# Optimization experiments

Hardware: AMD Instinct MI355X
Metric: run time of the kernel (lower is better)

Reference implementation:

```python
import jax, jax.numpy as jnp
import numpy as np

C = 1024
R = 4            # reduction
A = 10           # num_adapters
LN_EPS = 1e-5
THRESHOLDS = np.array([1/9, 1/7, 1/5, 1/3, 1.0, 3.0, 5.0, 7.0, 9.0], dtype=np.float32)


def setup_inputs() -> dict:
    key = jax.random.key(0)
    k_feat, k_ar, k_w1, k_w2 = jax.random.split(key, 4)
    B, NA, H, W = 2, 3, 64, 64
    Cr = C // R
    output_feat = jax.random.normal(k_feat, (B, C, H, W), jnp.float32)
    # aspect ratios in [0,10) so all 10 adapters get selected
    aspect_ratio = jax.random.uniform(k_ar, (B, NA, H, W), jnp.float32) * 10.0
    # LayerNorm params (torch default init: weight=1, bias=0), stacked over adapters
    ln_scale = jnp.ones((A, C), jnp.float32)
    ln_bias = jnp.zeros((A, C), jnp.float32)
    # kaiming_normal_ fan_out / relu: std = sqrt(2/fan_out); torch weight [out,in]
    # w1 here is [C, Cr] == torch weight [Cr, C].T, fan_out = Cr
    w1 = jax.random.normal(k_w1, (A, C, Cr), jnp.float32) * np.sqrt(2.0 / Cr)
    # w2 here is [Cr, C] == torch weight [C, Cr].T, fan_out = C
    w2 = jax.random.normal(k_w2, (A, Cr, C), jnp.float32) * np.sqrt(2.0 / C)
    return dict(output_feat=output_feat, aspect_ratio=aspect_ratio,
                ln_scale=ln_scale, ln_bias=ln_bias, w1=w1, w2=w2)


def reference(output_feat, aspect_ratio, ln_scale, ln_bias, w1, w2):
    B, Cc, H, W = output_feat.shape
    NA = aspect_ratio.shape[1]
    HW = H * W
    # tokens [N, C]
    x = output_feat.transpose(0, 2, 3, 1).reshape(-1, Cc)
    # shared LayerNorm normalization (per-adapter affine applied after)
    mu = jnp.mean(x, axis=-1, keepdims=True)
    var = jnp.var(x, axis=-1, keepdims=True)
    norm = (x - mu) * jax.lax.rsqrt(var + LN_EPS)              # [N, C]
    y = norm[None, :, :] * ln_scale[:, None, :] + ln_bias[:, None, :]  # [A, N, C]
    h = jax.nn.gelu(jnp.einsum('anc,acd->and', y, w1), approximate=False)
    adapter_out = jnp.einsum('and,adc->anc', h, w2)            # [A, N, C]
    adapter_out = adapter_out.reshape(A, B, HW, Cc)            # [A, B, HW, C]
    # per-anchor, per-pixel adapter index from aspect ratio vs thresholds
    thr = jnp.asarray(THRESHOLDS, dtype=aspect_ratio.dtype)
    ar = aspect_ratio.reshape(B, NA, HW)
    idx = jnp.sum(ar[..., None] > thr, axis=-1)                # [B, NA, HW] in [0, 9]
    # gather selected adapter output per (batch, anchor, pixel)
    b_idx = jnp.arange(B)[:, None, None]
    p_idx = jnp.arange(HW)[None, None, :]
    selected = adapter_out[idx, b_idx, p_idx]                  # [B, NA, HW, C]
    selected = selected.mean(axis=1).reshape(B, H, W, Cc).transpose(0, 3, 1, 2)
    return selected + output_feat
```

## Files before the change

### kernel.cpp

```cpp
#include <hip/hip_runtime.h>
#include <hip/hip_bf16.h>
#include <math.h>

#define C_DIM 1024
#define CR    256
#define A_N   10
#define NANCH 3
#define B_N   2
#define HW_N  4096
#define NTOK  (B_N*HW_N)
#define KG2   (A_N*CR)

typedef unsigned short ushort_t;
typedef __attribute__((ext_vector_type(4))) float f32x4;
typedef __attribute__((ext_vector_type(8))) short bf16x8;

__device__ __forceinline__ ushort_t f2bf(float x) {
    __hip_bfloat16 h = __float2bfloat16(x);
    return *reinterpret_cast<ushort_t*>(&h);
}
__device__ __forceinline__ float bf2f(ushort_t u) {
    return __uint_as_float(((unsigned)u) << 16);
}

__device__ __forceinline__ float fast_gelu(float x) {
    float t = x * x;
    float u = x * (-1.5957691216f - 0.0713548163f * t);
    float e = __expf(u);
    return x * __frcp_rn(1.0f + e);
}

__global__ __launch_bounds__(256) void prep_all(
    const float* __restrict__ w1, const float* __restrict__ w2,
    const float* __restrict__ ln_s, const float* __restrict__ ln_b,
    const float* __restrict__ feat, const float* __restrict__ ar,
    ushort_t* __restrict__ w1t, ushort_t* __restrict__ w2t,
    float* __restrict__ bias1, float* __restrict__ cs1,
    float* __restrict__ sumv, float* __restrict__ sumq,
    int* __restrict__ cnt, int* __restrict__ tokw, int* __restrict__ tokmap,
    ushort_t* __restrict__ featT) {
    __shared__ float lds[64][65];
    __shared__ float bb[8][64];
    __shared__ int lcnt[A_N], lpos[A_N], gbase[A_N];
    int id = blockIdx.x, tid = threadIdx.x;
    int lo = tid & 63, hi = tid >> 6;

    if (id < 640) {
        int d0 = (id & 3) * 64, c0 = ((id >> 2) & 15) * 64, a = id >> 6;
        #pragma unroll
        for (int i = 0; i < 16; i++) {
            int c_l = i * 4 + hi;
            lds[c_l][lo] = w1[((size_t)a * C_DIM + c0 + c_l) * CR + d0 + lo];
        }
        __syncthreads();
        {
            float s = 0.f, s2 = 0.f;
            #pragma unroll
            for (int cc = 0; cc < 16; cc++) {
                int c = hi * 16 + cc;
                float v = lds[c][lo];
                s  += v * ln_b[a * C_DIM + c0 + c];
                s2 += v * ln_s[a * C_DIM + c0 + c];
            }
            bb[hi][lo] = s;
            bb[hi + 4][lo] = s2;
        }
        float sc = ln_s[a * C_DIM + c0 + lo];
        #pragma unroll
        for (int i = 0; i < 16; i++) {
            int d_l = i * 4 + hi;
            w1t[((size_t)a * CR + d0 + d_l) * C_DIM + c0 + lo] = f2bf(lds[lo][d_l] * sc);
        }
        __syncthreads();
        if (hi == 0)
            atomicAdd(&bias1[a * CR + d0 + lo], bb[0][lo] + bb[1][lo] + bb[2][lo] + bb[3][lo]);
        else if (hi == 1)
            atomicAdd(&cs1[a * CR + d0 + lo], bb[4][lo] + bb[5][lo] + bb[6][lo] + bb[7][lo]);
    } else if (id < 1280) {
        int id2 = id - 640;
        int k0 = (id2 % 40) * 64, c0 = (id2 / 40) * 64;
        #pragma unroll
        for (int i = 0; i < 16; i++) {
            int k_l = i * 4 + hi;
            lds[k_l][lo] = w2[((size_t)k0 + k_l) * C_DIM + c0 + lo];
        }
        __syncthreads();
        #pragma unroll
        for (int i = 0; i < 16; i++) {
            int c_l = i * 4 + hi;
            w2t[((size_t)c0 + c_l) * KG2 + k0 + lo] = f2bf(lds[lo][c_l]);
        }
    } else if (id < 3328) {
        int id2 = id - 1280;
        int p0 = (id2 & 63) * 64, c0 = ((id2 >> 6) & 15) * 64, b = id2 >> 10;
        #pragma unroll
        for (int i = 0; i < 16; i++) {
            int c_l = i * 4 + hi;
            lds[c_l][lo] = feat[((size_t)b * C_DIM + c0 + c_l) * HW_N + p0 + lo];
        }
        __syncthreads();
        {
            float s = 0.f, s2 = 0.f;
            #pragma unroll
            for (int c = hi; c < 64; c += 4) {
                float v = lds[c][lo];
                s += v; s2 += v * v;
            }
            bb[hi][lo] = s; bb[hi + 4][lo] = s2;
        }
        __syncthreads();
        if (tid < 64) {
            float ss = bb[0][tid] + bb[1][tid] + bb[2][tid] + bb[3][tid];
            float qq = bb[4][tid] + bb[5][tid] + bb[6][tid] + bb[7][tid];
            int t = b * HW_N + p0 + tid;
            atomicAdd(&sumv[t], ss);
            atomicAdd(&sumq[t], qq);
        }
        int t_l = tid >> 3, cg = tid & 7;
        #pragma unroll
        for (int ii = 0; ii < 2; ii++) {
            int tl = ii * 32 + t_l;
            bf16x8 v;
            #pragma unroll
            for (int k = 0; k < 8; k++)
                v[k] = (short)f2bf(lds[cg * 8 + k][tl]);
            *(bf16x8*)(featT + (size_t)(b * HW_N + p0 + tl) * C_DIM + c0 + cg * 8) = v;
        }
    } else {
        if (tid < A_N) { lcnt[tid] = 0; lpos[tid] = 0; }
        __syncthreads();
        int t = (id - 3328) * 256 + tid;
        int b = t >> 12, p = t & (HW_N - 1);
        const float THR[9] = {1.0f/9.0f, 1.0f/7.0f, 0.2f, 1.0f/3.0f, 1.0f, 3.0f, 5.0f, 7.0f, 9.0f};
        int idxs[NANCH];
        #pragma unroll
        for (int na = 0; na < NANCH; na++) {
            float v = ar[(size_t)b * NANCH * HW_N + na * HW_N + p];
            int idx = 0;
            #pragma unroll
            for (int i = 0; i < 9; i++) idx += (v > THR[i]) ? 1 : 0;
            idxs[na] = idx;
        }
        int myA[NANCH], myC[NANCH], nmine = 0;
        #pragma unroll
        for (int j = 0; j < NANCH; j++) {
            bool first = true; int c3 = 0;
            #pragma unroll
            for (int k = 0; k < NANCH; k++) {
                if (idxs[k] == idxs[j]) { c3++; if (k < j) first = false; }
            }
            if (first) {
                myA[nmine] = idxs[j];
                myC[nmine] = c3;
                nmine++;
                atomicAdd(&lcnt[idxs[j]], 1);
            }
        }
        __syncthreads();
        if (tid < A_N) gbase[tid] = atomicAdd(&cnt[tid], lcnt[tid]);
        __syncthreads();
        for (int i = 0; i < NANCH; i++) {
            if (i < nmine) {
                int a2 = myA[i];
                int slot = atomicAdd(&lpos[a2], 1);
                int pos = gbase[a2] + slot;
                tokw[a2 * NTOK + pos] = t;
                tokmap[t * 3 + i] = pos | (a2 << 13) | (myC[i] << 17);
            } else {
                tokmap[t * 3 + i] = 0;
            }
        }
    }
}

__device__ __forceinline__ void gemm_core_ptrs(
    const ushort_t* const ap[4], const ushort_t* const bp[4],
    int K, ushort_t* As, ushort_t* Bs, f32x4 acc[4][4]) {
    const int tid = threadIdx.x;
    const int lane = tid & 63;
    const int w = tid >> 6;
    const int wr = w >> 1, wc = w & 1;
    const int lrow = lane & 15;
    const int quad = lane >> 4;
    const int swzr = lrow & 7;

    #pragma unroll
    for (int i = 0; i < 4; i++)
        #pragma unroll
        for (int j = 0; j < 4; j++)
            #pragma unroll
            for (int e = 0; e < 4; e++) acc[i][j][e] = 0.f;

    for (int k0 = 0; k0 < K; k0 += 64) {
        __syncthreads();
        #pragma unroll
        for (int i = 0; i < 4; i++) {
            __builtin_amdgcn_global_load_lds(
                (__attribute__((address_space(1))) void*)(ap[i] + k0),
                (__attribute__((address_space(3))) void*)(As + (w * 32 + i * 8) * 64),
                16, 0, 0);
            __builtin_amdgcn_global_load_lds(
                (__attribute__((address_space(1))) void*)(bp[i] + k0),
                (__attribute__((address_space(3))) void*)(Bs + (w * 32 + i * 8) * 64),
                16, 0, 0);
        }
        __syncthreads();
        #pragma unroll
        for (int ks = 0; ks < 2; ks++) {
            const int cidx = ((ks * 4 + quad) ^ swzr) * 8;
            bf16x8 af[4], bfr[4];
            #pragma unroll
            for (int mt = 0; mt < 4; mt++)
                af[mt] = *(const bf16x8*)(As + (wr * 64 + mt * 16 + lrow) * 64 + cidx);
            #pragma unroll
            for (int nt = 0; nt < 4; nt++)
                bfr[nt] = *(const bf16x8*)(Bs + (wc * 64 + nt * 16 + lrow) * 64 + cidx);
            #pragma unroll
            for (int mt = 0; mt < 4; mt++)
                #pragma unroll
                for (int nt = 0; nt < 4; nt++)
                    acc[mt][nt] = __builtin_amdgcn_mfma_f32_16x16x32_bf16(af[mt], bfr[nt], acc[mt][nt], 0, 0, 0);
        }
    }
}

__device__ __forceinline__ void gemm_core_bk128(
    const ushort_t* const ap[4], const ushort_t* const bp[4],
    int K, ushort_t* As, ushort_t* Bs, f32x4 acc[4][4]) {
    const int tid = threadIdx.x;
    const int lane = tid & 63;
    const int w = tid >> 6;
    const int wr = w >> 1, wc = w & 1;
    const int lrow = lane & 15;
    const int quad = lane >> 4;
    const int swzr = lrow & 7;

    #pragma unroll
    for (int i = 0; i < 4; i++)
        #pragma unroll
        for (int j = 0; j < 4; j++)
            #pragma unroll
            for (int e = 0; e < 4; e++) acc[i][j][e] = 0.f;

    for (int k0 = 0; k0 < K; k0 += 128) {
        __syncthreads();
        #pragma unroll
        for (int p = 0; p < 2; p++) {
            #pragma unroll
            for (int i = 0; i < 4; i++) {
                __builtin_amdgcn_global_load_lds(
                    (__attribute__((address_space(1))) void*)(ap[i] + k0 + p * 64),
                    (__attribute__((address_space(3))) void*)(As + p * 8192 + (w * 32 + i * 8) * 64),
                    16, 0, 0);
                __builtin_amdgcn_global_load_lds(
                    (__attribute__((address_space(1))) void*)(bp[i] + k0 + p * 64),
                    (__attribute__((address_space(3))) void*)(Bs + p * 8192 + (w * 32 + i * 8) * 64),
                    16, 0, 0);
            }
        }
        __syncthreads();
        #pragma unroll
        for (int ks = 0; ks < 4; ks++) {
            const ushort_t* Ab = As + (ks >> 1) * 8192;
            const ushort_t* Bb = Bs + (ks >> 1) * 8192;
            const int cidx = (((ks & 1) * 4 + quad) ^ swzr) * 8;
            bf16x8 af[4], bfr[4];
            #pragma unroll
            for (int mt = 0; mt < 4; mt++)
                af[mt] = *(const bf16x8*)(Ab + (wr * 64 + mt * 16 + lrow) * 64 + cidx);
            #pragma unroll
            for (int nt = 0; nt < 4; nt++)
                bfr[nt] = *(const bf16x8*)(Bb + (wc * 64 + nt * 16 + lrow) * 64 + cidx);
            #pragma unroll
            for (int mt = 0; mt < 4; mt++)
                #pragma unroll
                for (int nt = 0; nt < 4; nt++)
                    acc[mt][nt] = __builtin_amdgcn_mfma_f32_16x16x32_bf16(af[mt], bfr[nt], acc[mt][nt], 0, 0, 0);
        }
    }
}

__global__ __launch_bounds__(256) void gemm1c(const ushort_t* __restrict__ featT,
                                              const ushort_t* __restrict__ w1t,
                                              const float* __restrict__ bias1,
                                              const float* __restrict__ cs1,
                                              const float* __restrict__ sumv,
                                              const float* __restrict__ sumq,
                                              const int* __restrict__ tokw,
                                              const int* __restrict__ cnt,
                                              ushort_t* __restrict__ Hc) {
    int a = blockIdx.z;
    int mcount = cnt[a];
    int m0 = blockIdx.y * 128;
    if (m0 >= mcount) return;
    int n0 = blockIdx.x * 128;
    int base = 0;
    for (int a2 = 0; a2 < a; a2++) base += cnt[a2];

    __shared__ __align__(16) ushort_t As[2 * 128 * 64];
    __shared__ __align__(16) ushort_t Bs[2 * 128 * 64];

    int tid = threadIdx.x, lane = tid & 63, w = tid >> 6;
    int lrow8 = lane >> 3;
    int scol = ((lane & 7) ^ lrow8) * 8;
    int srowl = w * 32 + lrow8;

    const ushort_t* ap[4];
    const ushort_t* bp[4];
    #pragma unroll
    for (int i = 0; i < 4; i++) {
        int rt = tokw[a * NTOK + m0 + srowl + i * 8] & (NTOK - 1);
        ap[i] = featT + (size_t)rt * C_DIM + scol;
        bp[i] = w1t + ((size_t)a * CR + n0 + srowl + i * 8) * C_DIM + scol;
    }

    f32x4 acc[4][4];
    gemm_core_bk128(ap, bp, C_DIM, As, Bs, acc);

    int wr = w >> 1, wc = w & 1, lrow = lane & 15, quad = lane >> 4;
    float bi[4], cs[4];
    #pragma unroll
    for (int nt = 0; nt < 4; nt++) {
        int col = a * CR + n0 + wc * 64 + nt * 16 + lrow;
        bi[nt] = bias1[col];
        cs[nt] = cs1[col];
    }
    #pragma unroll
    for (int mt = 0; mt < 4; mt++)
        #pragma unroll
        for (int r = 0; r < 4; r++) {
            int i_row = m0 + wr * 64 + mt * 16 + quad * 4 + r;
            bool live = i_row < mcount;
            int t = tokw[a * NTOK + i_row] & (NTOK - 1);
            float m = sumv[t] * (1.f / C_DIM);
            float q = sumq[t] * (1.f / C_DIM);
            float rn = rsqrtf(q - m * m + 1e-5f);
            #pragma unroll
            for (int nt = 0; nt < 4; nt++) {
                int col = n0 + wc * 64 + nt * 16 + lrow;
                float v = rn * (acc[mt][nt][r] - m * cs[nt]) + bi[nt];
                if (live)
                    Hc[(size_t)(base + i_row) * CR + col] = f2bf(fast_gelu(v));
            }
        }
}

__global__ __launch_bounds__(256) void gemm2c(const ushort_t* __restrict__ Hc,
                                              const ushort_t* __restrict__ w2t,
                                              const int* __restrict__ cnt,
                                              ushort_t* __restrict__ O) {
    int a = blockIdx.z;
    int mcount = cnt[a];
    int m0 = blockIdx.y * 128;
    if (m0 >= mcount) return;
    int n0 = blockIdx.x * 128;
    int base = 0;
    for (int a2 = 0; a2 < a; a2++) base += cnt[a2];

    __shared__ __align__(16) ushort_t As[128 * 64];
    __shared__ __align__(16) ushort_t Bs[128 * 64];

    int tid = threadIdx.x, lane = tid & 63, w = tid >> 6;
    int lrow8 = lane >> 3;
    int scol = ((lane & 7) ^ lrow8) * 8;
    int srowl = w * 32 + lrow8;

    const ushort_t* ap[4];
    const ushort_t* bp[4];
    #pragma unroll
    for (int i = 0; i < 4; i++) {
        ap[i] = Hc + (size_t)(base + m0 + srowl + i * 8) * CR + scol;
        bp[i] = w2t + (size_t)(n0 + srowl + i * 8) * KG2 + a * CR + scol;
    }

    f32x4 acc[4][4];
    gemm_core_ptrs(ap, bp, CR, As, Bs, acc);

    int wr = w >> 1, wc = w & 1, lrow = lane & 15, quad = lane >> 4;
    #pragma unroll
    for (int mt = 0; mt < 4; mt++)
        #pragma unroll
        for (int r = 0; r < 4; r++) {
            int i_row = m0 + wr * 64 + mt * 16 + quad * 4 + r;
            bool live = i_row < mcount;
            #pragma unroll
            for (int nt = 0; nt < 4; nt++) {
                int col = n0 + wc * 64 + nt * 16 + lrow;
                if (live)
                    O[(size_t)(base + i_row) * C_DIM + col] = f2bf(acc[mt][nt][r]);
            }
        }
}

__global__ __launch_bounds__(256) void finalk2(const ushort_t* __restrict__ O,
                                               const int* __restrict__ tokmap,
                                               const int* __restrict__ cnt,
                                               const float* __restrict__ feat,
                                               float* __restrict__ out) {
    int p0 = blockIdx.x * 64, c0 = blockIdx.y * 64, b = blockIdx.z;
    __shared__ float lds[64][65];
    __shared__ int pbase[A_N];
    int tid = threadIdx.x, lo = tid & 63, hi = tid >> 6;
    if (tid < A_N) {
        int s = 0;
        for (int k = 0; k < tid; k++) s += cnt[k];
        pbase[tid] = s;
    }
    __syncthreads();
    int t_l = tid >> 3, cg = tid & 7;
    #pragma unroll
    for (int ii = 0; ii < 2; ii++) {
        int tl = ii * 32 + t_l;
        int t = b * HW_N + p0 + tl;
        float val8[8];
        #pragma unroll
        for (int k = 0; k < 8; k++) val8[k] = 0.f;
        #pragma unroll
        for (int j = 0; j < 3; j++) {
            int e = tokmap[t * 3 + j];
            float wv = (float)(e >> 17) * (1.0f / 3.0f);
            int a2 = (e >> 13) & 15;
            int row = pbase[a2] + (e & 8191);
            bf16x8 v = *(const bf16x8*)(O + (size_t)row * C_DIM + c0 + cg * 8);
            #pragma unroll
            for (int k = 0; k < 8; k++)
                val8[k] += wv * bf2f((ushort_t)v[k]);
        }
        #pragma unroll
        for (int k = 0; k < 8; k++)
            lds[tl][cg * 8 + k] = val8[k];
    }
    __syncthreads();
    #pragma unroll
    for (int i = 0; i < 16; i++) {
        int c_l = i * 4 + hi;
        size_t o = ((size_t)b * C_DIM + c0 + c_l) * HW_N + p0 + lo;
        out[o] = lds[lo][c_l] + feat[o];
    }
}

extern "C" void kernel_launch(void* const* d_in, const int* in_sizes, int n_in,
                              void* d_out, int out_size, void* d_ws, size_t ws_size,
                              hipStream_t stream) {
    (void)in_sizes; (void)n_in; (void)out_size; (void)ws_size;
    const float* feat = (const float*)d_in[0];
    const float* ar   = (const float*)d_in[1];
    const float* ln_s = (const float*)d_in[2];
    const float* ln_b = (const float*)d_in[3];
    const float* w1   = (const float*)d_in[4];
    const float* w2   = (const float*)d_in[5];
    float* out = (float*)d_out;
    char* ws = (char*)d_ws;

    float*    bias1  = (float*)(ws + 0);
    float*    cs1    = (float*)(ws + 10240);
    int*      cnt    = (int*)(ws + 20480);
    float*    sumv   = (float*)(ws + 20736);
    float*    sumq   = (float*)(ws + 53504);
    const size_t ZERO_BYTES = 86272;
    int*      tokmap = (int*)(ws + 86272);
    int*      tokw   = (int*)(ws + 184576);
    ushort_t* w1t    = (ushort_t*)(ws + 512256);
    ushort_t* w2t    = (ushort_t*)(ws + 5755136);
    ushort_t* featT  = (ushort_t*)(ws + 10998016);
    ushort_t* Hc     = (ushort_t*)(ws + 27775232);
    ushort_t* O      = (ushort_t*)(ws + 40423680);

    dim3 blk(256);
    hipMemsetAsync(ws, 0, ZERO_BYTES, stream);
    prep_all<<<dim3(3360), blk, 0, stream>>>(w1, w2, ln_s, ln_b, feat, ar,
                                             w1t, w2t, bias1, cs1, sumv, sumq,
                                             cnt, tokw, tokmap, featT);
    gemm1c<<<dim3(2, 64, A_N), blk, 0, stream>>>(featT, w1t, bias1, cs1, sumv, sumq,
                                                 tokw, cnt, Hc);
    gemm2c<<<dim3(8, 64, A_N), blk, 0, stream>>>(Hc, w2t, cnt, O);
    finalk2<<<dim3(64, 16, B_N), blk, 0, stream>>>(O, tokmap, cnt, feat, out);
}
```

Baseline: 95.42 us.

## Replace global atomics with partial-sum buffers and single-block token bucketing; drop memset

Token-to-adapter bucketing now runs in one block that loops over all tokens with only shared-memory atomics, which removes the global counter atomics. Per-token LayerNorm sums and per-column bias/colsum terms are written as 16 partial slots per row or column instead of being accumulated with global atomicAdd. gemm1c reduces those partials into shared memory in its epilogue. The hipMemsetAsync launch goes away, and the partial buffers alias the O buffer, which is written only later. The risk is that the serial single block becomes a long tail inside prep_all, since it walks 8192 tokens alone.

```diff
diff --git a/kernel.cpp b/kernel.cpp
--- a/kernel.cpp
+++ b/kernel.cpp
@@ -35,18 +35,55 @@
     const float* __restrict__ ln_s, const float* __restrict__ ln_b,
     const float* __restrict__ feat, const float* __restrict__ ar,
     ushort_t* __restrict__ w1t, ushort_t* __restrict__ w2t,
-    float* __restrict__ bias1, float* __restrict__ cs1,
-    float* __restrict__ sumv, float* __restrict__ sumq,
+    float* __restrict__ bias1P, float* __restrict__ cs1P,
+    float* __restrict__ sums,
     int* __restrict__ cnt, int* __restrict__ tokw, int* __restrict__ tokmap,
     ushort_t* __restrict__ featT) {
     __shared__ float lds[64][65];
     __shared__ float bb[8][64];
-    __shared__ int lcnt[A_N], lpos[A_N], gbase[A_N];
+    __shared__ int lpos[A_N];
     int id = blockIdx.x, tid = threadIdx.x;
     int lo = tid & 63, hi = tid >> 6;
 
-    if (id < 640) {
-        int d0 = (id & 3) * 64, c0 = ((id >> 2) & 15) * 64, a = id >> 6;
+    if (id == 0) {
+        if (tid < A_N) lpos[tid] = 0;
+        __syncthreads();
+        const float THR[9] = {1.0f/9.0f, 1.0f/7.0f, 0.2f, 1.0f/3.0f, 1.0f, 3.0f, 5.0f, 7.0f, 9.0f};
+        for (int it = 0; it < NTOK / 256; ++it) {
+            int t = it * 256 + tid;
+            int b = t >> 12, p = t & (HW_N - 1);
+            int idxs[NANCH];
+            #pragma unroll
+            for (int na = 0; na < NANCH; na++) {
+                float v = ar[(size_t)b * NANCH * HW_N + na * HW_N + p];
+                int idx = 0;
+                #pragma unroll
+                for (int i = 0; i < 9; i++) idx += (v > THR[i]) ? 1 : 0;
+                idxs[na] = idx;
+            }
+            #pragma unroll
+            for (int j = 0; j < NANCH; j++) {
+                bool first = true; int c3 = 0;
+                #pragma unroll
+                for (int k = 0; k < NANCH; k++) {
+                    if (idxs[k] == idxs[j]) { c3++; if (k < j) first = false; }
+                }
+                int e = 0;
+                if (first) {
+                    int a2 = idxs[j];
+                    int pos = atomicAdd(&lpos[a2], 1);
+                    tokw[a2 * NTOK + pos] = t;
+                    e = pos | (a2 << 13) | (c3 << 17);
+                }
+                tokmap[t * 3 + j] = e;
+            }
+        }
+        __syncthreads();
+        if (tid < A_N) cnt[tid] = lpos[tid];
+    } else if (id < 641) {
+        int id2 = id - 1;
+        int d0 = (id2 & 3) * 64, c0idx = (id2 >> 2) & 15, a = id2 >> 6;
+        int c0 = c0idx * 64;
         #pragma unroll
         for (int i = 0; i < 16; i++) {
             int c_l = i * 4 + hi;
@@ -73,11 +110,13 @@
         }
         __syncthreads();
         if (hi == 0)
-            atomicAdd(&bias1[a * CR + d0 + lo], bb[0][lo] + bb[1][lo] + bb[2][lo] + bb[3][lo]);
+            bias1P[(size_t)(a * CR + d0 + lo) * 16 + c0idx] =
+                bb[0][lo] + bb[1][lo] + bb[2][lo] + bb[3][lo];
         else if (hi == 1)
-            atomicAdd(&cs1[a * CR + d0 + lo], bb[4][lo] + bb[5][lo] + bb[6][lo] + bb[7][lo]);
-    } else if (id < 1280) {
-        int id2 = id - 640;
+            cs1P[(size_t)(a * CR + d0 + lo) * 16 + c0idx] =
+                bb[4][lo] + bb[5][lo] + bb[6][lo] + bb[7][lo];
+    } else if (id < 1281) {
+        int id2 = id - 641;
         int k0 = (id2 % 40) * 64, c0 = (id2 / 40) * 64;
         #pragma unroll
         for (int i = 0; i < 16; i++) {
@@ -90,9 +129,10 @@
             int c_l = i * 4 + hi;
             w2t[((size_t)c0 + c_l) * KG2 + k0 + lo] = f2bf(lds[lo][c_l]);
         }
-    } else if (id < 3328) {
-        int id2 = id - 1280;
-        int p0 = (id2 & 63) * 64, c0 = ((id2 >> 6) & 15) * 64, b = id2 >> 10;
+    } else {
+        int id2 = id - 1281;
+        int p0 = (id2 & 63) * 64, c0idx = (id2 >> 6) & 15, b = id2 >> 10;
+        int c0 = c0idx * 64;
         #pragma unroll
         for (int i = 0; i < 16; i++) {
             int c_l = i * 4 + hi;
@@ -113,8 +153,8 @@
             float ss = bb[0][tid] + bb[1][tid] + bb[2][tid] + bb[3][tid];
             float qq = bb[4][tid] + bb[5][tid] + bb[6][tid] + bb[7][tid];
             int t = b * HW_N + p0 + tid;
-            atomicAdd(&sumv[t], ss);
-            atomicAdd(&sumq[t], qq);
+            sums[(size_t)t * 32 + c0idx] = ss;
+            sums[(size_t)t * 32 + 16 + c0idx] = qq;
         }
         int t_l = tid >> 3, cg = tid & 7;
         #pragma unroll
@@ -125,50 +165,6 @@
             for (int k = 0; k < 8; k++)
                 v[k] = (short)f2bf(lds[cg * 8 + k][tl]);
             *(bf16x8*)(featT + (size_t)(b * HW_N + p0 + tl) * C_DIM + c0 + cg * 8) = v;
-        }
-    } else {
-        if (tid < A_N) { lcnt[tid] = 0; lpos[tid] = 0; }
-        __syncthreads();
-        int t = (id - 3328) * 256 + tid;
-        int b = t >> 12, p = t & (HW_N - 1);
-        const float THR[9] = {1.0f/9.0f, 1.0f/7.0f, 0.2f, 1.0f/3.0f, 1.0f, 3.0f, 5.0f, 7.0f, 9.0f};
-        int idxs[NANCH];
-        #pragma unroll
-        for (int na = 0; na < NANCH; na++) {
-            float v = ar[(size_t)b * NANCH * HW_N + na * HW_N + p];
-            int idx = 0;
-            #pragma unroll
-            for (int i = 0; i < 9; i++) idx += (v > THR[i]) ? 1 : 0;
-            idxs[na] = idx;
-        }
-        int myA[NANCH], myC[NANCH], nmine = 0;
-        #pragma unroll
-        for (int j = 0; j < NANCH; j++) {
-            bool first = true; int c3 = 0;
-            #pragma unroll
-            for (int k = 0; k < NANCH; k++) {
-                if (idxs[k] == idxs[j]) { c3++; if (k < j) first = false; }
-            }
-            if (first) {
-                myA[nmine] = idxs[j];
-                myC[nmine] = c3;
-                nmine++;
-                atomicAdd(&lcnt[idxs[j]], 1);
-            }
-        }
-        __syncthreads();
-        if (tid < A_N) gbase[tid] = atomicAdd(&cnt[tid], lcnt[tid]);
-        __syncthreads();
-        for (int i = 0; i < NANCH; i++) {
-            if (i < nmine) {
-                int a2 = myA[i];
-                int slot = atomicAdd(&lpos[a2], 1);
-                int pos = gbase[a2] + slot;
-                tokw[a2 * NTOK + pos] = t;
-                tokmap[t * 3 + i] = pos | (a2 << 13) | (myC[i] << 17);
-            } else {
-                tokmap[t * 3 + i] = 0;
-            }
         }
     }
 }
@@ -282,10 +278,9 @@
 
 __global__ __launch_bounds__(256) void gemm1c(const ushort_t* __restrict__ featT,
                                               const ushort_t* __restrict__ w1t,
-                                              const float* __restrict__ bias1,
-                                              const float* __restrict__ cs1,
-                                              const float* __restrict__ sumv,
-                                              const float* __restrict__ sumq,
+                                              const float* __restrict__ bias1P,
+                                              const float* __restrict__ cs1P,
+                                              const float* __restrict__ sums,
                                               const int* __restrict__ tokw,
                                               const int* __restrict__ cnt,
                                               ushort_t* __restrict__ Hc) {
@@ -299,6 +294,7 @@
 
     __shared__ __align__(16) ushort_t As[2 * 128 * 64];
     __shared__ __align__(16) ushort_t Bs[2 * 128 * 64];
+    __shared__ float rowM[128], rowR[128], colB[128], colC[128];
 
     int tid = threadIdx.x, lane = tid & 63, w = tid >> 6;
     int lrow8 = lane >> 3;
@@ -317,24 +313,44 @@
     f32x4 acc[4][4];
     gemm_core_bk128(ap, bp, C_DIM, As, Bs, acc);
 
+    if (tid < 128) {
+        int t = tokw[a * NTOK + m0 + tid] & (NTOK - 1);
+        const f32x4* sp = (const f32x4*)(sums + (size_t)t * 32);
+        f32x4 sv = sp[0] + sp[1] + sp[2] + sp[3];
+        f32x4 sq = sp[4] + sp[5] + sp[6] + sp[7];
+        float m = (sv[0] + sv[1] + sv[2] + sv[3]) * (1.f / C_DIM);
+        float q = (sq[0] + sq[1] + sq[2] + sq[3]) * (1.f / C_DIM);
+        rowM[tid] = m;
+        rowR[tid] = rsqrtf(q - m * m + 1e-5f);
+    } else {
+        int j = tid - 128;
+        size_t col = (size_t)(a * CR + n0 + j);
+        const f32x4* bp4 = (const f32x4*)(bias1P + col * 16);
+        const f32x4* cp4 = (const f32x4*)(cs1P + col * 16);
+        f32x4 b4 = bp4[0] + bp4[1] + bp4[2] + bp4[3];
+        f32x4 c4 = cp4[0] + cp4[1] + cp4[2] + cp4[3];
+        colB[j] = b4[0] + b4[1] + b4[2] + b4[3];
+        colC[j] = c4[0] + c4[1] + c4[2] + c4[3];
+    }
+    __syncthreads();
+
     int wr = w >> 1, wc = w & 1, lrow = lane & 15, quad = lane >> 4;
     float bi[4], cs[4];
     #pragma unroll
     for (int nt = 0; nt < 4; nt++) {
-        int col = a * CR + n0 + wc * 64 + nt * 16 + lrow;
-        bi[nt] = bias1[col];
-        cs[nt] = cs1[col];
+        int cl = wc * 64 + nt * 16 + lrow;
+        bi[nt] = colB[cl];
+        cs[nt] = colC[cl];
     }
     #pragma unroll
     for (int mt = 0; mt < 4; mt++)
         #pragma unroll
         for (int r = 0; r < 4; r++) {
-            int i_row = m0 + wr * 64 + mt * 16 + quad * 4 + r;
+            int rl = wr * 64 + mt * 16 + quad * 4 + r;
+            int i_row = m0 + rl;
             bool live = i_row < mcount;
-            int t = tokw[a * NTOK + i_row] & (NTOK - 1);
-            float m = sumv[t] * (1.f / C_DIM);
-            float q = sumq[t] * (1.f / C_DIM);
-            float rn = rsqrtf(q - m * m + 1e-5f);
+            float m = rowM[rl];
+            float rn = rowR[rl];
             #pragma unroll
             for (int nt = 0; nt < 4; nt++) {
                 int col = n0 + wc * 64 + nt * 16 + lrow;
@@ -452,26 +468,23 @@
     float* out = (float*)d_out;
     char* ws = (char*)d_ws;
 
-    float*    bias1  = (float*)(ws + 0);
-    float*    cs1    = (float*)(ws + 10240);
-    int*      cnt    = (int*)(ws + 20480);
-    float*    sumv   = (float*)(ws + 20736);
-    float*    sumq   = (float*)(ws + 53504);
-    const size_t ZERO_BYTES = 86272;
-    int*      tokmap = (int*)(ws + 86272);
-    int*      tokw   = (int*)(ws + 184576);
-    ushort_t* w1t    = (ushort_t*)(ws + 512256);
-    ushort_t* w2t    = (ushort_t*)(ws + 5755136);
-    ushort_t* featT  = (ushort_t*)(ws + 10998016);
-    ushort_t* Hc     = (ushort_t*)(ws + 27775232);
-    ushort_t* O      = (ushort_t*)(ws + 40423680);
+    int*      cnt    = (int*)(ws + 0);
+    int*      tokmap = (int*)(ws + 64);
+    int*      tokw   = (int*)(ws + 98368);
+    ushort_t* w1t    = (ushort_t*)(ws + 426048);
+    ushort_t* w2t    = (ushort_t*)(ws + 5668928);
+    ushort_t* featT  = (ushort_t*)(ws + 10911808);
+    ushort_t* Hc     = (ushort_t*)(ws + 27689024);
+    ushort_t* O      = (ushort_t*)(ws + 40337472);
+    float*    sums   = (float*)O;
+    float*    bias1P = (float*)((char*)O + 1048576);
+    float*    cs1P   = (float*)((char*)O + 1212416);
 
     dim3 blk(256);
-    hipMemsetAsync(ws, 0, ZERO_BYTES, stream);
-    prep_all<<<dim3(3360), blk, 0, stream>>>(w1, w2, ln_s, ln_b, feat, ar,
-                                             w1t, w2t, bias1, cs1, sumv, sumq,
+    prep_all<<<dim3(3329), blk, 0, stream>>>(w1, w2, ln_s, ln_b, feat, ar,
+                                             w1t, w2t, bias1P, cs1P, sums,
                                              cnt, tokw, tokmap, featT);
-    gemm1c<<<dim3(2, 64, A_N), blk, 0, stream>>>(featT, w1t, bias1, cs1, sumv, sumq,
+    gemm1c<<<dim3(2, 64, A_N), blk, 0, stream>>>(featT, w1t, bias1P, cs1P, sums,
                                                  tokw, cnt, Hc);
     gemm2c<<<dim3(8, 64, A_N), blk, 0, stream>>>(Hc, w2t, cnt, O);
     finalk2<<<dim3(64, 16, B_N), blk, 0, stream>>>(O, tokmap, cnt, feat, out);
```

Result: slower. 115.5 us (+21.1%).
